# Optimization experiments

Measured on AMD Instinct MI355X. Metric: run time of the kernel, lower is better.

Reference implementation:

```python
import jax, jax.numpy as jnp
import numpy as np

N, F, F_, H = 8192, 512, 64, 8
NEG = -1e10

def setup_inputs() -> dict:
    key = jax.random.key(0)
    k1, k2, k3, k4 = jax.random.split(key, 4)
    X = jax.random.normal(k1, (N, F), dtype=jnp.float32)
    A = jax.random.randint(k2, (N, N), 0, 2).astype(jnp.float32)  # dense 0/1 adjacency
    kernels = jax.random.normal(k3, (H, F, F_), dtype=jnp.float32) * 0.05
    attn_kernels = jax.random.normal(k4, (H, 2 * F_), dtype=jnp.float32) * 0.05
    return {"X": X, "A": A, "kernels": kernels, "attn_kernels": attn_kernels}

def reference(X, A, kernels, attn_kernels):
    # Per-head linear transform: [H, N, F_]
    WX = jnp.einsum('nf,hfo->hno', X, kernels)
    a1 = attn_kernels[:, :F_]   # [H, F_] acts on source (row) node
    a2 = attn_kernels[:, F_:]   # [H, F_] acts on target (col) node
    # score[h,i,j] = a1_h . WX[h,i] + a2_h . WX[h,j]  (outer sum, no N^2*2F_ tensor)
    s1 = jnp.einsum('hno,ho->hn', WX, a1)  # [H, N]
    s2 = jnp.einsum('hno,ho->hn', WX, a2)  # [H, N]
    scores = s1[:, :, None] + s2[:, None, :]  # [H, N, N]
    # adjacency mask: A==0 -> -1e10 (note: original has no LeakyReLU)
    masked = jnp.where(A[None, :, :] == 0.0, scores + NEG, scores)
    attn = jax.nn.softmax(masked, axis=-1)  # [H, N, N]
    # dropout is identity at inference (Keras Dropout without training=True)
    feats = jnp.einsum('hnm,hmo->hno', attn, WX)  # [H, N, F_]
    feats = jax.nn.relu(feats)  # concat reduction applies activation per head
    out = jnp.transpose(feats, (1, 0, 2)).reshape(N, H * F_)  # concat heads
    return out
```

## Files before the change

kernel.cpp:

```cpp
#include <hip/hip_runtime.h>
#include <cstdint>

#define NN 8192
#define FF 512
#define FO 64
#define NH 8
#define LDYE 520
#define YPART (8192 * 520)
#define SPLITK 3


typedef __attribute__((ext_vector_type(8))) __bf16 bf16x8;
typedef __attribute__((ext_vector_type(4))) float f32x4;

__device__ __forceinline__ unsigned short f2bf(float f) {
    unsigned int u = __float_as_uint(f);
    u += 0x7fffu + ((u >> 16) & 1u);
    return (unsigned short)(u >> 16);
}

__device__ __forceinline__ void gload16(const void* g, void* l) {
    __builtin_amdgcn_global_load_lds(
        (const __attribute__((address_space(1))) unsigned int*)g,
        (__attribute__((address_space(3))) unsigned int*)l,
        16, 0, 0);
}

__global__ __launch_bounds__(256) void k_convA8(const float* __restrict__ A,
                                                unsigned char* __restrict__ Ab) {
    const size_t gid = (size_t)blockIdx.x * 256 + threadIdx.x;
    const int row = (int)(gid & 63);
    const int k16 = (int)((gid >> 6) & 511);
    const int rt = (int)(gid >> 15);
    const uint4* src = (const uint4*)(A + (((size_t)(rt * 64 + row)) << 13) + k16 * 16);
    uint4 f0 = src[0], f1 = src[1], f2 = src[2], f3 = src[3];
#define PK8(v) (((v.x >> 22) & 0x38u) | (((v.y >> 22) & 0x38u) << 8) | \
                (((v.z >> 22) & 0x38u) << 16) | (((v.w >> 22) & 0x38u) << 24))
    uint4 o = {PK8(f0), PK8(f1), PK8(f2), PK8(f3)};
#undef PK8
    *(uint4*)(Ab + (gid << 4)) = o;
}

__global__ __launch_bounds__(256) void k_prep(const float* __restrict__ X,
                                              const float* __restrict__ Kw,
                                              unsigned short* __restrict__ Xb,
                                              unsigned short* __restrict__ Ktb) {
    const int b = blockIdx.x;
    const int t = threadIdx.x;
    if (b < 2048) {
        size_t base = ((size_t)b * 256 + t) * 8;
        float4 a = *(const float4*)(X + base);
        float4 c = *(const float4*)(X + base + 4);
        ushort4 o0, o1;
        o0.x = f2bf(a.x); o0.y = f2bf(a.y); o0.z = f2bf(a.z); o0.w = f2bf(a.w);
        o1.x = f2bf(c.x); o1.y = f2bf(c.y); o1.z = f2bf(c.z); o1.w = f2bf(c.w);
        *(ushort4*)(Xb + base) = o0;
        *(ushort4*)(Xb + base + 4) = o1;
    } else {
        int h = b - 2048;
        for (int e = t; e < FF * FO; e += 256) {
            int o = e >> 9, f = e & 511;
            Ktb[(size_t)h * FF * FO + e] = f2bf(Kw[(size_t)h * FF * FO + (size_t)f * FO + o]);
        }
    }
}

union WxSmem {
    struct { unsigned short Xs[4096]; unsigned short Ks[2048]; } s;
    unsigned char Vs[64][144];
};

__global__ __launch_bounds__(256) void k_wx(const unsigned short* __restrict__ Xb,
                                            const unsigned short* __restrict__ Ktb,
                                            const float* __restrict__ Aw,
                                            unsigned char* __restrict__ Vt) {
    __shared__ WxSmem sm;
    const int t = threadIdx.x;
    const int n0 = blockIdx.x * 128;
    const int h = blockIdx.y;
    const int lane = t & 63, w = t >> 6;
    const int quad = lane >> 4, l15 = lane & 15;

    const unsigned short* xS0 = Xb + (size_t)(n0 + (t & 127)) * FF + (t >> 7) * 8;
    const unsigned short* xS1 = Xb + (size_t)(n0 + ((t + 256) & 127)) * FF + ((t + 256) >> 7) * 8;
    unsigned short* xD0 = sm.s.Xs + t * 8;
    unsigned short* xD1 = sm.s.Xs + (t + 256) * 8;
    const unsigned short* kS = Ktb + (size_t)h * FF * FO + (size_t)(t & 63) * FF + (t >> 6) * 8;
    unsigned short* kD = sm.s.Ks + t * 8;

    const bf16x8* aF[2];
    const bf16x8* bF[4];
    for (int i = 0; i < 2; ++i)
        aF[i] = (const bf16x8*)(sm.s.Xs + (size_t)(quad * 128 + w * 32 + i * 16 + l15) * 8);
    for (int j = 0; j < 4; ++j)
        bF[j] = (const bf16x8*)(sm.s.Ks + (size_t)(quad * 64 + j * 16 + l15) * 8);

    f32x4 acc[2][4] = {};
    for (int f0 = 0; f0 < FF; f0 += 32) {
        gload16(xS0 + f0, xD0);
        gload16(xS1 + f0, xD1);
        gload16(kS + f0, kD);
        __syncthreads();
        bf16x8 av[2], bv[4];
        for (int i = 0; i < 2; ++i) av[i] = aF[i][0];
        for (int j = 0; j < 4; ++j) bv[j] = bF[j][0];
        for (int i = 0; i < 2; ++i)
            for (int j = 0; j < 4; ++j)
                acc[i][j] = __builtin_amdgcn_mfma_f32_16x16x32_bf16(av[i], bv[j], acc[i][j], 0, 0, 0);
        __syncthreads();
    }

    float a2v[4];
    for (int j = 0; j < 4; ++j) a2v[j] = Aw[h * 128 + 64 + j * 16 + l15];
    float ex[2][4];
    for (int i = 0; i < 2; ++i)
        for (int r = 0; r < 4; ++r) {
            float p = acc[i][0][r] * a2v[0] + acc[i][1][r] * a2v[1]
                    + acc[i][2][r] * a2v[2] + acc[i][3][r] * a2v[3];
            p += __shfl_xor(p, 1);
            p += __shfl_xor(p, 2);
            p += __shfl_xor(p, 4);
            p += __shfl_xor(p, 8);
            ex[i][r] = __expf(p);
        }

    for (int i = 0; i < 2; ++i)
        for (int j = 0; j < 4; ++j) {
            int rowb = w * 32 + i * 16 + quad * 4;
            int col = j * 16 + l15;
            unsigned u = __builtin_amdgcn_cvt_pk_fp8_f32(
                ex[i][0] * acc[i][j][0], ex[i][1] * acc[i][j][1], 0, false);
            u = __builtin_amdgcn_cvt_pk_fp8_f32(
                ex[i][2] * acc[i][j][2], ex[i][3] * acc[i][j][3], (int)u, true);
            *(unsigned*)&sm.Vs[col][rowb] = u;
        }
    __syncthreads();
    for (int j2 = 0; j2 < 2; ++j2) {
        int vid = t + j2 * 256;
        int o = vid >> 3, k16o = vid & 7;
        size_t H = (size_t)((n0 >> 4) + k16o) * 640 + h * 64 + o;
        *(uint4*)(Vt + (H << 4)) = *(const uint4*)&sm.Vs[o][k16o * 16];
    }
    if (l15 == 0) {
        for (int i = 0; i < 2; ++i)
            for (int r = 0; r < 4; ++r) {
                int row = w * 32 + i * 16 + quad * 4 + r;
                unsigned u = __builtin_amdgcn_cvt_pk_fp8_f32(ex[i][r], ex[i][r], 0, false);
                size_t H = (size_t)((n0 >> 4) + (row >> 4)) * 640 + 512 + h;
                Vt[(H << 4) + (row & 15)] = (unsigned char)(u & 0xff);
            }
    }
}

__global__ __launch_bounds__(256, 5) void k_gemm(const unsigned char* __restrict__ Ab,
                                                 const unsigned char* __restrict__ Vt,
                                                 float* __restrict__ Y) {
    __shared__ unsigned char As[4096];
    __shared__ unsigned char Bs[10240];
    const int t = threadIdx.x;
    const int id = blockIdx.x;
    const int xcd = id & 7;
    const int u = id >> 3;
    const int ct = u & 3;
    const int rp = ((u >> 2) << 3) | xcd;
    const int rt = rp & 127;
    const int part = rp >> 7;
    const int ks0 = (part * 128) / SPLITK;
    const int ks1 = ((part + 1) * 128) / SPLITK;

    const unsigned char* aS = Ab + ((size_t)rt << 19) + (size_t)t * 16;
    unsigned char* aD = As + t * 16;
    const int g1 = t + 256, g2 = t + 512;
    const unsigned char* bS0 = Vt + (size_t)((t / 160) * 10240 + (ct * 160 + t % 160) * 16);
    const unsigned char* bS1 = Vt + (size_t)((g1 / 160) * 10240 + (ct * 160 + g1 % 160) * 16);
    const unsigned char* bS2 = Vt + (size_t)((g2 / 160) * 10240 + (ct * 160 + g2 % 160) * 16);
    unsigned char* bD0 = Bs + t * 16;
    unsigned char* bD1 = Bs + g1 * 16;
    unsigned char* bD2 = Bs + g2 * 16;

    const int lane = t & 63;
    const int w = t >> 6;
    const int wm = w >> 1, wn = w & 1;
    const int quad = lane >> 4, l15 = lane & 15;

    int aOff[2], bOff[5];
    for (int i = 0; i < 2; ++i)
        aOff[i] = (quad >> 1) * 1024 + (quad & 1) * 8 + (wm * 32 + i * 16 + l15) * 16;
    for (int j = 0; j < 5; ++j)
        bOff[j] = (quad >> 1) * 2560 + (quad & 1) * 8 + (wn * 80 + j * 16 + l15) * 16;

    f32x4 acc[2][5] = {};

    for (int ks = ks0; ks < ks1; ++ks) {
        const size_t koA = (size_t)ks << 12;
        const size_t koB = (size_t)ks * 40960;
        gload16(aS + koA, aD);
        gload16(bS0 + koB, bD0);
        gload16(bS1 + koB, bD1);
        if (t < 128) gload16(bS2 + koB, bD2);
        __syncthreads();
#pragma unroll
        for (int h2 = 0; h2 < 2; ++h2) {
            long long av[2], bv[5];
            for (int i = 0; i < 2; ++i)
                av[i] = *(const long long*)(As + aOff[i] + h2 * 2048);
            for (int j = 0; j < 5; ++j)
                bv[j] = *(const long long*)(Bs + bOff[j] + h2 * 5120);
            for (int i = 0; i < 2; ++i)
                for (int j = 0; j < 5; ++j)
                    acc[i][j] = __builtin_amdgcn_mfma_f32_16x16x32_fp8_fp8(
                        av[i], bv[j], acc[i][j], 0, 0, 0);
        }
        __syncthreads();
    }

    float* Yp = Y + (size_t)part * YPART;
    for (int i = 0; i < 2; ++i) {
        int row = rt * 64 + wm * 32 + i * 16 + quad * 4;
        for (int j = 0; j < 5; ++j) {
            int col = ct * 160 + wn * 80 + j * 16 + l15;
            if (col < 520) {
                for (int r = 0; r < 4; ++r)
                    Yp[(size_t)(row + r) * LDYE + col] = acc[i][j][r];
            }
        }
    }
}

__global__ __launch_bounds__(256) void k_epi(const float* __restrict__ Y,
                                             float* __restrict__ out) {
    int idx = blockIdx.x * 256 + threadIdx.x;
    int n = idx >> 7;
    int c = (idx & 127) * 4;
    int h = c >> 6;
    float4 u = {0.f, 0.f, 0.f, 0.f};
    float den = 0.f;
    const float* yp = Y + (size_t)n * LDYE;
#pragma unroll
    for (int p = 0; p < SPLITK; ++p) {
        float4 v = *(const float4*)(yp + c);
        u.x += v.x; u.y += v.y; u.z += v.z; u.w += v.w;
        den += yp[512 + h];
        yp += (size_t)YPART;
    }
    float inv = 1.0f / den;
    float4 o;
    o.x = fmaxf(u.x * inv, 0.f);
    o.y = fmaxf(u.y * inv, 0.f);
    o.z = fmaxf(u.z * inv, 0.f);
    o.w = fmaxf(u.w * inv, 0.f);
    *(float4*)(out + (size_t)n * 512 + c) = o;
}

extern "C" void kernel_launch(void* const* d_in, const int* in_sizes, int n_in,
                              void* d_out, int out_size, void* d_ws, size_t ws_size,
                              hipStream_t stream) {
    const float* X  = (const float*)d_in[0];
    const float* A  = (const float*)d_in[1];
    const float* Kw = (const float*)d_in[2];
    const float* Aw = (const float*)d_in[3];
    float* out = (float*)d_out;
    char* ws = (char*)d_ws;
    unsigned char* Ab = (unsigned char*)ws;
    unsigned char* Vt = (unsigned char*)(ws + (size_t)67108864);
    float* Yb = (float*)(ws + (size_t)67108864 + (size_t)5242880);
    unsigned short* Xb = (unsigned short*)Yb;
    unsigned short* Ktb = Xb + (size_t)NN * FF;

    k_convA8<<<dim3(16384), dim3(256), 0, stream>>>(A, Ab);
    k_prep<<<dim3(2056), dim3(256), 0, stream>>>(X, Kw, Xb, Ktb);
    k_wx<<<dim3(64, 8), dim3(256), 0, stream>>>(Xb, Ktb, Aw, Vt);
    k_gemm<<<dim3(1536), dim3(256), 0, stream>>>(Ab, Vt, Yb);
    k_epi<<<dim3(4096), dim3(256), 0, stream>>>(Yb, out);
}
```

Before: 509.3 us.

## Use 16x16x128 scaled FP8 MFMA with doubled K-step in split-K GEMM

Replaces the 16x16x32 FP8 MFMA in the adjacency-times-features GEMM with the MI355X scaled 16x16x128 f8f6f4 MFMA, using unit scales (0x7f). Each K iteration now loads twice as much A and B data into LDS, which halves the number of iterations and barriers, and LDS reads become 16-byte vector loads. The LDS footprint doubles to about 28KB per block, which may lower occupancy under launch_bounds(256,5). Correctness depends on the LDS fragment layout matching the operand layout the new instruction expects.

```diff
diff --git a/kernel.cpp b/kernel.cpp
--- a/kernel.cpp
+++ b/kernel.cpp
@@ -12,6 +12,8 @@
 
 typedef __attribute__((ext_vector_type(8))) __bf16 bf16x8;
 typedef __attribute__((ext_vector_type(4))) float f32x4;
+typedef __attribute__((ext_vector_type(4))) int i32x4;
+typedef __attribute__((ext_vector_type(8))) int i32x8;
 
 __device__ __forceinline__ unsigned short f2bf(float f) {
     unsigned int u = __float_as_uint(f);
@@ -155,8 +157,8 @@
 __global__ __launch_bounds__(256, 5) void k_gemm(const unsigned char* __restrict__ Ab,
                                                  const unsigned char* __restrict__ Vt,
                                                  float* __restrict__ Y) {
-    __shared__ unsigned char As[4096];
-    __shared__ unsigned char Bs[10240];
+    __shared__ unsigned char As[8192];
+    __shared__ unsigned char Bs[20480];
     const int t = threadIdx.x;
     const int id = blockIdx.x;
     const int xcd = id & 7;
@@ -165,18 +167,20 @@
     const int rp = ((u >> 2) << 3) | xcd;
     const int rt = rp & 127;
     const int part = rp >> 7;
-    const int ks0 = (part * 128) / SPLITK;
-    const int ks1 = ((part + 1) * 128) / SPLITK;
+    const int ks0 = (part * 64) / SPLITK;
+    const int ks1 = ((part + 1) * 64) / SPLITK;
 
     const unsigned char* aS = Ab + ((size_t)rt << 19) + (size_t)t * 16;
-    unsigned char* aD = As + t * 16;
-    const int g1 = t + 256, g2 = t + 512;
-    const unsigned char* bS0 = Vt + (size_t)((t / 160) * 10240 + (ct * 160 + t % 160) * 16);
-    const unsigned char* bS1 = Vt + (size_t)((g1 / 160) * 10240 + (ct * 160 + g1 % 160) * 16);
-    const unsigned char* bS2 = Vt + (size_t)((g2 / 160) * 10240 + (ct * 160 + g2 % 160) * 16);
-    unsigned char* bD0 = Bs + t * 16;
-    unsigned char* bD1 = Bs + g1 * 16;
-    unsigned char* bD2 = Bs + g2 * 16;
+    unsigned char* aD0 = As + t * 16;
+    unsigned char* aD1 = As + t * 16 + 4096;
+    const unsigned char* bS[5];
+    unsigned char* bD[5];
+#pragma unroll
+    for (int j = 0; j < 5; ++j) {
+        int g = t + 256 * j;
+        bS[j] = Vt + (size_t)((g / 160) * 640 + ct * 160 + (g % 160)) * 16;
+        bD[j] = Bs + g * 16;
+    }
 
     const int lane = t & 63;
     const int w = t >> 6;
@@ -184,32 +188,39 @@
     const int quad = lane >> 4, l15 = lane & 15;
 
     int aOff[2], bOff[5];
-    for (int i = 0; i < 2; ++i)
-        aOff[i] = (quad >> 1) * 1024 + (quad & 1) * 8 + (wm * 32 + i * 16 + l15) * 16;
+#pragma unroll
+    for (int i = 0; i < 2; ++i)
+        aOff[i] = quad * 2048 + (wm * 32 + i * 16 + l15) * 16;
+#pragma unroll
     for (int j = 0; j < 5; ++j)
-        bOff[j] = (quad >> 1) * 2560 + (quad & 1) * 8 + (wn * 80 + j * 16 + l15) * 16;
+        bOff[j] = quad * 5120 + (wn * 80 + j * 16 + l15) * 16;
 
     f32x4 acc[2][5] = {};
 
     for (int ks = ks0; ks < ks1; ++ks) {
-        const size_t koA = (size_t)ks << 12;
-        const size_t koB = (size_t)ks * 40960;
-        gload16(aS + koA, aD);
-        gload16(bS0 + koB, bD0);
-        gload16(bS1 + koB, bD1);
-        if (t < 128) gload16(bS2 + koB, bD2);
-        __syncthreads();
-#pragma unroll
-        for (int h2 = 0; h2 < 2; ++h2) {
-            long long av[2], bv[5];
-            for (int i = 0; i < 2; ++i)
-                av[i] = *(const long long*)(As + aOff[i] + h2 * 2048);
-            for (int j = 0; j < 5; ++j)
-                bv[j] = *(const long long*)(Bs + bOff[j] + h2 * 5120);
-            for (int i = 0; i < 2; ++i)
-                for (int j = 0; j < 5; ++j)
-                    acc[i][j] = __builtin_amdgcn_mfma_f32_16x16x32_fp8_fp8(
-                        av[i], bv[j], acc[i][j], 0, 0, 0);
+        const size_t koA = (size_t)ks << 13;
+        const size_t koB = (size_t)ks * 81920;
+        gload16(aS + koA, aD0);
+        gload16(aS + koA + 4096, aD1);
+#pragma unroll
+        for (int j = 0; j < 5; ++j) gload16(bS[j] + koB, bD[j]);
+        __syncthreads();
+        i32x8 av[2];
+#pragma unroll
+        for (int i = 0; i < 2; ++i) {
+            i32x4 lo = *(const i32x4*)(As + aOff[i]);
+            i32x4 hi = *(const i32x4*)(As + aOff[i] + 1024);
+            av[i] = __builtin_shufflevector(lo, hi, 0, 1, 2, 3, 4, 5, 6, 7);
+        }
+#pragma unroll
+        for (int j = 0; j < 5; ++j) {
+            i32x4 lo = *(const i32x4*)(Bs + bOff[j]);
+            i32x4 hi = *(const i32x4*)(Bs + bOff[j] + 2560);
+            i32x8 bv = __builtin_shufflevector(lo, hi, 0, 1, 2, 3, 4, 5, 6, 7);
+            acc[0][j] = __builtin_amdgcn_mfma_scale_f32_16x16x128_f8f6f4(
+                av[0], bv, acc[0][j], 0, 0, 0, 0x7f7f7f7f, 0, 0x7f7f7f7f);
+            acc[1][j] = __builtin_amdgcn_mfma_scale_f32_16x16x128_f8f6f4(
+                av[1], bv, acc[1][j], 0, 0, 0, 0x7f7f7f7f, 0, 0x7f7f7f7f);
         }
         __syncthreads();
     }
```

Result: no change. 503.6 us (-1.1%).
